# Kernel tuning notes

Hardware: AMD Instinct MI355X
Metric: run time of the kernel (lower is better)

Reference implementation:

```python
import jax, jax.numpy as jnp
import numpy as np

TOPK = 2
NORM_TOPK = True
SCALE = 1.0
EPS = 1e-9


def setup_inputs() -> dict:
    key = jax.random.key(0)
    ks = jax.random.split(key, 9)
    h, i, E = 2048, 1024, 16
    std = 0.02
    return {
        "x": jax.random.normal(ks[0], (1, 2048, h), jnp.float32),
        "Wr": jax.random.normal(ks[1], (E, h), jnp.float32) * std,
        "bias": jnp.zeros((E,), jnp.float32),
        "Wg": jax.random.normal(ks[2], (E, h, i), jnp.float32) * std,
        "Wu": jax.random.normal(ks[3], (E, h, i), jnp.float32) * std,
        "Wd": jax.random.normal(ks[4], (E, i, h), jnp.float32) * std,
        "sWg": jax.random.normal(ks[5], (h, i), jnp.float32) * std,
        "sWu": jax.random.normal(ks[6], (h, i), jnp.float32) * std,
        "sWd": jax.random.normal(ks[7], (i, h), jnp.float32) * std,
    }


def reference(x, Wr, bias, Wg, Wu, Wd, sWg, sWu, sWd):
    b, s, h = x.shape
    E = Wr.shape[0]
    xt = x.reshape(b * s, h)  # [T, h]

    # Router: softmax over expert logits, then top-k
    logits = xt @ Wr.T + bias  # [T, E]
    probs = jax.nn.softmax(logits, axis=-1)
    topk_val, topk_idx = jax.lax.top_k(probs, TOPK)  # [T, K]
    if NORM_TOPK:
        w = topk_val / (jnp.sum(topk_val, axis=-1, keepdims=True) + EPS)
    else:
        w = topk_val
    w = w * SCALE

    # Dense per-expert SwiGLU (mathematically identical to gather/scatter dispatch)
    g = jnp.einsum('th,ehi->tei', xt, Wg)  # [T, E, i]
    u = jnp.einsum('th,ehi->tei', xt, Wu)
    y = jnp.einsum('tei,eih->teh', jax.nn.silu(g) * u, Wd)  # [T, E, h]

    # Combine: out[t] = sum_k w[t,k] * y[t, idx[t,k]]
    oh = jax.nn.one_hot(topk_idx, E, dtype=x.dtype)  # [T, K, E]
    routed = jnp.einsum('tke,tk,teh->th', oh, w, y)

    # Shared expert (SwiGLU)
    shared = (jax.nn.silu(xt @ sWg) * (xt @ sWu)) @ sWd

    return (routed + shared).reshape(b, s, h)
```

## Files before the change

### kernel.cpp

```cpp
#include <hip/hip_runtime.h>
#include <hip/hip_bf16.h>

#define T_TOK 2048
#define HDIM  2048
#define IDIM  1024
#define NE    16
#define NEX   17
#define NASSIGN (T_TOK*3)
#define TM    64

#define G1_NCT 16
#define G2_NCT 32
#define G1_NWG (TM*G1_NCT)
#define G2_NWG (TM*G2_NCT)

typedef __attribute__((ext_vector_type(8))) short bf16x8;
typedef __attribute__((ext_vector_type(4))) float f32x4;

__device__ __forceinline__ unsigned short f2bf(float f) {
    union { float f; unsigned u; } v; v.f = f;
    unsigned r = v.u + 0x7fffu + ((v.u >> 16) & 1u);
    return (unsigned short)(r >> 16);
}
__device__ __forceinline__ unsigned pack2f(float a, float b) {
    __hip_bfloat162 h = __float22bfloat162_rn(float2{a, b});
    unsigned r;
    __builtin_memcpy(&r, &h, 4);
    return r;
}
__device__ __forceinline__ float fidx(const float4& v, int j) {
    return ((const float*)&v)[j];
}
__device__ __forceinline__ int SW(int r) { return (r ^ (r >> 2)) & 7; }
__device__ __forceinline__ int lds_off(int row, int kelem) {
    return (row << 7) + ((((kelem >> 3) ^ SW(row))) << 4) + ((kelem & 7) << 1);
}
__device__ __forceinline__ f32x4 mfma16(bf16x8 a, bf16x8 b, f32x4 c) {
    return __builtin_amdgcn_mfma_f32_16x16x32_bf16(a, b, c, 0, 0, 0);
}

__global__ __launch_bounds__(256) void k_cvt(const float* __restrict__ x,
                                             unsigned short* __restrict__ xbf) {
    int i = blockIdx.x * 256 + threadIdx.x;
    float4 v = ((const float4*)x)[i];
    uint2 p{pack2f(v.x, v.y), pack2f(v.z, v.w)};
    ((uint2*)xbf)[i] = p;
}

__global__ void k_router(const float* __restrict__ x, const float* __restrict__ Wr,
                         const float* __restrict__ bias, float* __restrict__ wtok,
                         int* __restrict__ idxtok, int* __restrict__ counts) {
    int t = blockIdx.x;
    int lane = threadIdx.x & 63;
    int wave = threadIdx.x >> 6;
    __shared__ float lg[NE];
    const float4* xr = (const float4*)(x + (size_t)t * HDIM);
    for (int e = wave; e < NE; e += 4) {
        const float4* wr = (const float4*)(Wr + (size_t)e * HDIM);
        float s = 0.f;
        for (int j = lane; j < HDIM / 4; j += 64) {
            float4 a = xr[j], b = wr[j];
            s += a.x*b.x + a.y*b.y + a.z*b.z + a.w*b.w;
        }
        #pragma unroll
        for (int d = 32; d; d >>= 1) s += __shfl_xor(s, d);
        if (lane == 0) lg[e] = s + bias[e];
    }
    __syncthreads();
    if (threadIdx.x == 0) {
        float m = lg[0];
        #pragma unroll
        for (int e = 1; e < NE; e++) m = fmaxf(m, lg[e]);
        float p[NE]; float S = 0.f;
        #pragma unroll
        for (int e = 0; e < NE; e++) { p[e] = expf(lg[e] - m); S += p[e]; }
        int i0 = 0;
        #pragma unroll
        for (int e = 1; e < NE; e++) if (p[e] > p[i0]) i0 = e;
        int i1 = (i0 == 0) ? 1 : 0;
        for (int e = 0; e < NE; e++) if (e != i0 && p[e] > p[i1]) i1 = e;
        float v0 = p[i0] / S, v1 = p[i1] / S;
        float wsum = v0 + v1 + 1e-9f;
        wtok[t*2+0] = v0 / wsum;
        wtok[t*2+1] = v1 / wsum;
        idxtok[t*2+0] = i0;
        idxtok[t*2+1] = i1;
        atomicAdd(&counts[i0], 1);
        atomicAdd(&counts[i1], 1);
    }
}

__global__ void k_scan(const int* __restrict__ counts, int* __restrict__ offs,
                       int* __restrict__ cursor, int4* __restrict__ tiles) {
    if (threadIdx.x == 0) {
        int acc = 0;
        for (int e = 0; e < NEX; e++) {
            offs[e] = acc; cursor[e] = acc;
            acc += (e < NE) ? counts[e] : T_TOK;
        }
        offs[NEX] = acc;
        int nt = 0;
        for (int e = 0; e < NEX; e++) {
            for (int r = offs[e]; r < offs[e+1]; r += 128) {
                tiles[nt] = int4{r, min(128, offs[e+1] - r), e, 0};
                nt++;
            }
        }
        for (; nt < TM; nt++) tiles[nt] = int4{0, 0, 0, 0};
    }
}

__global__ void k_scatter(const int* __restrict__ idxtok, const float* __restrict__ wtok,
                          int* __restrict__ cursor, const int* __restrict__ offs,
                          int* __restrict__ rows, float* __restrict__ wrow) {
    int t = blockIdx.x * blockDim.x + threadIdx.x;
    if (t >= T_TOK) return;
    #pragma unroll
    for (int k = 0; k < 2; k++) {
        int e = idxtok[t*2+k];
        int pos = atomicAdd(&cursor[e], 1);
        rows[pos] = t;
        wrow[pos] = wtok[t*2+k];
    }
    int p16 = offs[NE] + t;
    rows[p16] = t;
    wrow[p16] = 1.0f;
}

__global__ __launch_bounds__(512) void k_gemm1(
        const unsigned short* __restrict__ xbf,
        const float* __restrict__ Wg, const float* __restrict__ Wu,
        const float* __restrict__ sWg, const float* __restrict__ sWu,
        const int4* __restrict__ tiles, const int* __restrict__ rows,
        const float* __restrict__ wrow, unsigned short* __restrict__ act) {
    int bid = blockIdx.x;
    int wg = (bid & 7) * (G1_NWG >> 3) + (bid >> 3);
    int ti = wg & (TM - 1);
    int ct = wg >> 6;

    int4 tl = tiles[ti];
    int nrows = tl.y;
    if (nrows == 0) return;
    int rs = tl.x, e = tl.z;
    const float* wgp = (e < NE) ? Wg + (size_t)e * HDIM * IDIM : sWg;
    const float* wup = (e < NE) ? Wu + (size_t)e * HDIM * IDIM : sWu;
    int n0 = ct * 64;

    __shared__ unsigned short As[2][128 * 64];
    __shared__ unsigned short Bs[2][64 * 64];
    __shared__ unsigned short Us[2][64 * 64];
    __shared__ int rloc[128];

    int tid = threadIdx.x;
    if (tid < 128) rloc[tid] = rows[rs + min(tid, nrows - 1)];
    __syncthreads();

    int arow = tid >> 2;
    int akc  = (tid & 3) << 4;
    const unsigned short* asrc = xbf + (size_t)rloc[arow] * HDIM + akc;
    int n4 = (tid & 15) << 2;
    int kb = (tid >> 4) << 1;
    const float* gsrc = wgp + (size_t)kb * IDIM + n0 + n4;
    const float* usrc = wup + (size_t)kb * IDIM + n0 + n4;

    int l = tid & 63, w = tid >> 6;
    int wr = (w >> 2) << 6;
    int wc = (w & 3) << 4;
    int fr = l & 15;
    int fk = (l >> 4) << 3;

    uint4 aR0, aR1;
    float4 gR0, gR1, uR0, uR1;

    #define G1_LOAD(K0) do { \
        aR0 = *(const uint4*)(asrc + (K0)); \
        aR1 = *(const uint4*)(asrc + (K0) + 8); \
        gR0 = *(const float4*)(gsrc + (size_t)(K0) * IDIM); \
        gR1 = *(const float4*)(gsrc + (size_t)(K0) * IDIM + IDIM); \
        uR0 = *(const float4*)(usrc + (size_t)(K0) * IDIM); \
        uR1 = *(const float4*)(usrc + (size_t)(K0) * IDIM + IDIM); \
    } while (0)

    #define G1_WRITE(B) do { \
        *(uint4*)((char*)As[B] + lds_off(arow, akc))     = aR0; \
        *(uint4*)((char*)As[B] + lds_off(arow, akc + 8)) = aR1; \
        _Pragma("unroll") \
        for (int i = 0; i < 4; ++i) { \
            int n = n4 + i; \
            *(unsigned*)((char*)Bs[B] + lds_off(n, kb)) = pack2f(fidx(gR0,i), fidx(gR1,i)); \
            *(unsigned*)((char*)Us[B] + lds_off(n, kb)) = pack2f(fidx(uR0,i), fidx(uR1,i)); \
        } \
    } while (0)

    f32x4 accg[4] = {}, accu[4] = {};
    const int NK = HDIM / 64;

    G1_LOAD(0);
    G1_WRITE(0);
    G1_LOAD(64);
    __syncthreads();

    for (int k = 0; k < NK; ++k) {
        int buf = k & 1;
        #pragma unroll
        for (int kh = 0; kh < 2; ++kh) {
            int kk = (kh << 5) + fk;
            bf16x8 a[4], bg, bu;
            #pragma unroll
            for (int m = 0; m < 4; ++m)
                a[m] = *(const bf16x8*)((const char*)As[buf] + lds_off(wr + m * 16 + fr, kk));
            bg = *(const bf16x8*)((const char*)Bs[buf] + lds_off(wc + fr, kk));
            bu = *(const bf16x8*)((const char*)Us[buf] + lds_off(wc + fr, kk));
            #pragma unroll
            for (int m = 0; m < 4; ++m) {
                accg[m] = mfma16(a[m], bg, accg[m]);
                accu[m] = mfma16(a[m], bu, accu[m]);
            }
        }
        if (k + 1 < NK) {
            G1_WRITE(buf ^ 1);
            if (k + 2 < NK) G1_LOAD((k + 2) * 64);
            __syncthreads();
        }
    }

    int crow = (l >> 4) << 2;
    int ccol = l & 15;
    #pragma unroll
    for (int m = 0; m < 4; ++m) {
        #pragma unroll
        for (int reg = 0; reg < 4; ++reg) {
            int r = wr + m * 16 + crow + reg;
            if (r < nrows) {
                float wv = wrow[rs + r];
                float g = accg[m][reg], u = accu[m][reg];
                act[(size_t)(rs + r) * IDIM + n0 + wc + ccol] =
                    f2bf(g / (1.f + __expf(-g)) * u * wv);
            }
        }
    }
}

__global__ __launch_bounds__(512) void k_gemm2(
        const unsigned short* __restrict__ act,
        const float* __restrict__ Wd, const float* __restrict__ sWd,
        const int4* __restrict__ tiles, const int* __restrict__ rows,
        float* __restrict__ out) {
    int bid = blockIdx.x;
    int wg = (bid & 7) * (G2_NWG >> 3) + (bid >> 3);
    int ti = wg & (TM - 1);
    int ct = wg >> 6;

    int4 tl = tiles[ti];
    int nrows = tl.y;
    if (nrows == 0) return;
    int rs = tl.x, e = tl.z;
    const float* wdp = (e < NE) ? Wd + (size_t)e * IDIM * HDIM : sWd;
    int n0 = ct * 64;

    __shared__ unsigned short As[2][128 * 64];
    __shared__ unsigned short Bs[2][64 * 64];
    __shared__ int rloc[128];

    int tid = threadIdx.x;
    if (tid < 128) rloc[tid] = rows[rs + min(tid, nrows - 1)];
    __syncthreads();

    int arow = tid >> 2;
    int akc  = (tid & 3) << 4;
    const unsigned short* asrc = act + (size_t)(rs + min(arow, nrows - 1)) * IDIM + akc;
    int n4 = (tid & 15) << 2;
    int kb = (tid >> 4) << 1;
    const float* dsrc = wdp + (size_t)kb * HDIM + n0 + n4;

    int l = tid & 63, w = tid >> 6;
    int wr = (w >> 2) << 6;
    int wc = (w & 3) << 4;
    int fr = l & 15;
    int fk = (l >> 4) << 3;

    uint4 aR0, aR1;
    float4 dR0, dR1;

    #define G2_LOAD(K0) do { \
        aR0 = *(const uint4*)(asrc + (K0)); \
        aR1 = *(const uint4*)(asrc + (K0) + 8); \
        dR0 = *(const float4*)(dsrc + (size_t)(K0) * HDIM); \
        dR1 = *(const float4*)(dsrc + (size_t)(K0) * HDIM + HDIM); \
    } while (0)

    #define G2_WRITE(B) do { \
        *(uint4*)((char*)As[B] + lds_off(arow, akc))     = aR0; \
        *(uint4*)((char*)As[B] + lds_off(arow, akc + 8)) = aR1; \
        _Pragma("unroll") \
        for (int i = 0; i < 4; ++i) { \
            int n = n4 + i; \
            *(unsigned*)((char*)Bs[B] + lds_off(n, kb)) = pack2f(fidx(dR0,i), fidx(dR1,i)); \
        } \
    } while (0)

    f32x4 acc[4] = {};
    const int NK = IDIM / 64;

    G2_LOAD(0);
    G2_WRITE(0);
    G2_LOAD(64);
    __syncthreads();

    for (int k = 0; k < NK; ++k) {
        int buf = k & 1;
        #pragma unroll
        for (int kh = 0; kh < 2; ++kh) {
            int kk = (kh << 5) + fk;
            bf16x8 a[4], b;
            #pragma unroll
            for (int m = 0; m < 4; ++m)
                a[m] = *(const bf16x8*)((const char*)As[buf] + lds_off(wr + m * 16 + fr, kk));
            b = *(const bf16x8*)((const char*)Bs[buf] + lds_off(wc + fr, kk));
            #pragma unroll
            for (int m = 0; m < 4; ++m)
                acc[m] = mfma16(a[m], b, acc[m]);
        }
        if (k + 1 < NK) {
            G2_WRITE(buf ^ 1);
            if (k + 2 < NK) G2_LOAD((k + 2) * 64);
            __syncthreads();
        }
    }

    int crow = (l >> 4) << 2;
    int ccol = l & 15;
    #pragma unroll
    for (int m = 0; m < 4; ++m) {
        #pragma unroll
        for (int reg = 0; reg < 4; ++reg) {
            int r = wr + m * 16 + crow + reg;
            if (r < nrows) {
                atomicAdd(&out[(size_t)rloc[r] * HDIM + n0 + wc + ccol], acc[m][reg]);
            }
        }
    }
}

extern "C" void kernel_launch(void* const* d_in, const int* in_sizes, int n_in,
                              void* d_out, int out_size, void* d_ws, size_t ws_size,
                              hipStream_t stream) {
    const float* x    = (const float*)d_in[0];
    const float* Wr   = (const float*)d_in[1];
    const float* bias = (const float*)d_in[2];
    const float* Wg   = (const float*)d_in[3];
    const float* Wu   = (const float*)d_in[4];
    const float* Wd   = (const float*)d_in[5];
    const float* sWg  = (const float*)d_in[6];
    const float* sWu  = (const float*)d_in[7];
    const float* sWd  = (const float*)d_in[8];
    float* out = (float*)d_out;

    char* p = (char*)d_ws;
    int*   counts = (int*)p;                 p += 256;
    int*   offs   = (int*)p;                 p += 256;
    int*   cursor = (int*)p;                 p += 256;
    int4*  tiles  = (int4*)p;                p += TM * sizeof(int4);
    int*   idxtok = (int*)p;                 p += (size_t)T_TOK * 2 * sizeof(int);
    float* wtok   = (float*)p;               p += (size_t)T_TOK * 2 * sizeof(float);
    int*   rows   = (int*)p;                 p += (size_t)NASSIGN * sizeof(int);
    float* wrow   = (float*)p;               p += (size_t)NASSIGN * sizeof(float);
    unsigned short* act = (unsigned short*)p; p += (size_t)NASSIGN * IDIM * sizeof(unsigned short);
    unsigned short* xbf = (unsigned short*)p;

    hipMemsetAsync(counts, 0, 256, stream);
    hipMemsetAsync(d_out, 0, (size_t)out_size * sizeof(float), stream);

    k_cvt<<<dim3(T_TOK * HDIM / 1024), dim3(256), 0, stream>>>(x, xbf);
    k_router<<<dim3(T_TOK), dim3(256), 0, stream>>>(x, Wr, bias, wtok, idxtok, counts);
    k_scan<<<dim3(1), dim3(64), 0, stream>>>(counts, offs, cursor, tiles);
    k_scatter<<<dim3((T_TOK + 255) / 256), dim3(256), 0, stream>>>(idxtok, wtok, cursor, offs, rows, wrow);
    k_gemm1<<<dim3(G1_NWG), dim3(512), 0, stream>>>(xbf, Wg, Wu, sWg, sWu, tiles, rows, wrow, act);
    k_gemm2<<<dim3(G2_NWG), dim3(512), 0, stream>>>(act, Wd, sWd, tiles, rows, out);
}
```

Baseline: 318.6 us.

## Load activation tiles directly into LDS with global_load_lds and manual waitcnt pipelining

```diff
diff --git a/kernel.cpp b/kernel.cpp
--- a/kernel.cpp
+++ b/kernel.cpp
@@ -17,6 +17,11 @@
 typedef __attribute__((ext_vector_type(8))) short bf16x8;
 typedef __attribute__((ext_vector_type(4))) float f32x4;
 
+#define WAITVM(N) asm volatile("s_waitcnt vmcnt(" #N ")" ::: "memory")
+#define WAITLGKM  asm volatile("s_waitcnt lgkmcnt(0)" ::: "memory")
+#define SCHEDB    __builtin_amdgcn_sched_barrier(0)
+#define BARRIER   __builtin_amdgcn_s_barrier()
+
 __device__ __forceinline__ unsigned short f2bf(float f) {
     union { float f; unsigned u; } v; v.f = f;
     unsigned r = v.u + 0x7fffu + ((v.u >> 16) & 1u);
@@ -37,6 +42,11 @@
 }
 __device__ __forceinline__ f32x4 mfma16(bf16x8 a, bf16x8 b, f32x4 c) {
     return __builtin_amdgcn_mfma_f32_16x16x32_bf16(a, b, c, 0, 0, 0);
+}
+__device__ __forceinline__ void gload_lds16(const void* g, void* lds) {
+    __builtin_amdgcn_global_load_lds(
+        (const __attribute__((address_space(1))) unsigned*)g,
+        (__attribute__((address_space(3))) unsigned*)lds, 16, 0, 0);
 }
 
 __global__ __launch_bounds__(256) void k_cvt(const float* __restrict__ x,
@@ -155,35 +165,37 @@
     if (tid < 128) rloc[tid] = rows[rs + min(tid, nrows - 1)];
     __syncthreads();
 
-    int arow = tid >> 2;
-    int akc  = (tid & 3) << 4;
-    const unsigned short* asrc = xbf + (size_t)rloc[arow] * HDIM + akc;
+    int l = tid & 63, w = tid >> 6;
+    int ar0 = w * 8 + (l >> 3);
+    int ar1 = 64 + ar0;
+    const unsigned short* asrc0 = xbf + (size_t)rloc[ar0] * HDIM + (((l & 7) ^ SW(ar0)) << 3);
+    const unsigned short* asrc1 = xbf + (size_t)rloc[ar1] * HDIM + (((l & 7) ^ SW(ar1)) << 3);
+
     int n4 = (tid & 15) << 2;
     int kb = (tid >> 4) << 1;
     const float* gsrc = wgp + (size_t)kb * IDIM + n0 + n4;
     const float* usrc = wup + (size_t)kb * IDIM + n0 + n4;
 
-    int l = tid & 63, w = tid >> 6;
     int wr = (w >> 2) << 6;
     int wc = (w & 3) << 4;
     int fr = l & 15;
     int fk = (l >> 4) << 3;
 
-    uint4 aR0, aR1;
     float4 gR0, gR1, uR0, uR1;
 
-    #define G1_LOAD(K0) do { \
-        aR0 = *(const uint4*)(asrc + (K0)); \
-        aR1 = *(const uint4*)(asrc + (K0) + 8); \
+    #define G1_LOADW(K0) do { \
         gR0 = *(const float4*)(gsrc + (size_t)(K0) * IDIM); \
         gR1 = *(const float4*)(gsrc + (size_t)(K0) * IDIM + IDIM); \
         uR0 = *(const float4*)(usrc + (size_t)(K0) * IDIM); \
         uR1 = *(const float4*)(usrc + (size_t)(K0) * IDIM + IDIM); \
     } while (0)
 
-    #define G1_WRITE(B) do { \
-        *(uint4*)((char*)As[B] + lds_off(arow, akc))     = aR0; \
-        *(uint4*)((char*)As[B] + lds_off(arow, akc + 8)) = aR1; \
+    #define G1_GLOADA(K0, B) do { \
+        gload_lds16(asrc0 + (K0), (char*)As[B] + w * 1024); \
+        gload_lds16(asrc1 + (K0), (char*)As[B] + 8192 + w * 1024); \
+    } while (0)
+
+    #define G1_WRITEW(B) do { \
         _Pragma("unroll") \
         for (int i = 0; i < 4; ++i) { \
             int n = n4 + i; \
@@ -194,14 +206,29 @@
 
     f32x4 accg[4] = {}, accu[4] = {};
     const int NK = HDIM / 64;
-
-    G1_LOAD(0);
-    G1_WRITE(0);
-    G1_LOAD(64);
-    __syncthreads();
+    const int KLAST = (NK - 1) * 64;
+
+    G1_LOADW(0);
+    G1_GLOADA(0, 0);
+    SCHEDB;
+    WAITVM(2);
+    G1_WRITEW(0);
+    G1_LOADW(64);
+    SCHEDB;
+    WAITVM(4);
+    WAITLGKM;
+    BARRIER;
 
     for (int k = 0; k < NK; ++k) {
         int buf = k & 1;
+        int kA = min((k + 1) * 64, KLAST);
+        int kW = min((k + 2) * 64, KLAST);
+        G1_GLOADA(kA, buf ^ 1);
+        SCHEDB;
+        WAITVM(2);
+        G1_WRITEW(buf ^ 1);
+        G1_LOADW(kW);
+        SCHEDB;
         #pragma unroll
         for (int kh = 0; kh < 2; ++kh) {
             int kk = (kh << 5) + fk;
@@ -217,12 +244,11 @@
                 accu[m] = mfma16(a[m], bu, accu[m]);
             }
         }
-        if (k + 1 < NK) {
-            G1_WRITE(buf ^ 1);
-            if (k + 2 < NK) G1_LOAD((k + 2) * 64);
-            __syncthreads();
-        }
-    }
+        WAITVM(4);
+        WAITLGKM;
+        BARRIER;
+    }
+    WAITVM(0);
 
     int crow = (l >> 4) << 2;
     int ccol = l & 15;
@@ -239,6 +265,9 @@
             }
         }
     }
+    #undef G1_LOADW
+    #undef G1_GLOADA
+    #undef G1_WRITEW
 }
 
 __global__ __launch_bounds__(512) void k_gemm2(
@@ -266,32 +295,34 @@
     if (tid < 128) rloc[tid] = rows[rs + min(tid, nrows - 1)];
     __syncthreads();
 
-    int arow = tid >> 2;
-    int akc  = (tid & 3) << 4;
-    const unsigned short* asrc = act + (size_t)(rs + min(arow, nrows - 1)) * IDIM + akc;
+    int l = tid & 63, w = tid >> 6;
+    int ar0 = w * 8 + (l >> 3);
+    int ar1 = 64 + ar0;
+    const unsigned short* asrc0 = act + (size_t)(rs + ar0) * IDIM + (((l & 7) ^ SW(ar0)) << 3);
+    const unsigned short* asrc1 = act + (size_t)(rs + ar1) * IDIM + (((l & 7) ^ SW(ar1)) << 3);
+
     int n4 = (tid & 15) << 2;
     int kb = (tid >> 4) << 1;
     const float* dsrc = wdp + (size_t)kb * HDIM + n0 + n4;
 
-    int l = tid & 63, w = tid >> 6;
     int wr = (w >> 2) << 6;
     int wc = (w & 3) << 4;
     int fr = l & 15;
     int fk = (l >> 4) << 3;
 
-    uint4 aR0, aR1;
     float4 dR0, dR1;
 
-    #define G2_LOAD(K0) do { \
-        aR0 = *(const uint4*)(asrc + (K0)); \
-        aR1 = *(const uint4*)(asrc + (K0) + 8); \
+    #define G2_LOADW(K0) do { \
         dR0 = *(const float4*)(dsrc + (size_t)(K0) * HDIM); \
         dR1 = *(const float4*)(dsrc + (size_t)(K0) * HDIM + HDIM); \
     } while (0)
 
-    #define G2_WRITE(B) do { \
-        *(uint4*)((char*)As[B] + lds_off(arow, akc))     = aR0; \
-        *(uint4*)((char*)As[B] + lds_off(arow, akc + 8)) = aR1; \
+    #define G2_GLOADA(K0, B) do { \
+        gload_lds16(asrc0 + (K0), (char*)As[B] + w * 1024); \
+        gload_lds16(asrc1 + (K0), (char*)As[B] + 8192 + w * 1024); \
+    } while (0)
+
+    #define G2_WRITEW(B) do { \
         _Pragma("unroll") \
         for (int i = 0; i < 4; ++i) { \
             int n = n4 + i; \
@@ -301,14 +332,29 @@
 
     f32x4 acc[4] = {};
     const int NK = IDIM / 64;
-
-    G2_LOAD(0);
-    G2_WRITE(0);
-    G2_LOAD(64);
-    __syncthreads();
+    const int KLAST = (NK - 1) * 64;
+
+    G2_LOADW(0);
+    G2_GLOADA(0, 0);
+    SCHEDB;
+    WAITVM(2);
+    G2_WRITEW(0);
+    G2_LOADW(64);
+    SCHEDB;
+    WAITVM(2);
+    WAITLGKM;
+    BARRIER;
 
     for (int k = 0; k < NK; ++k) {
         int buf = k & 1;
+        int kA = min((k + 1) * 64, KLAST);
+        int kW = min((k + 2) * 64, KLAST);
+        G2_GLOADA(kA, buf ^ 1);
+        SCHEDB;
+        WAITVM(2);
+        G2_WRITEW(buf ^ 1);
+        G2_LOADW(kW);
+        SCHEDB;
         #pragma unroll
         for (int kh = 0; kh < 2; ++kh) {
             int kk = (kh << 5) + fk;
@@ -321,12 +367,11 @@
             for (int m = 0; m < 4; ++m)
                 acc[m] = mfma16(a[m], b, acc[m]);
         }
-        if (k + 1 < NK) {
-            G2_WRITE(buf ^ 1);
-            if (k + 2 < NK) G2_LOAD((k + 2) * 64);
-            __syncthreads();
-        }
-    }
+        WAITVM(2);
+        WAITLGKM;
+        BARRIER;
+    }
+    WAITVM(0);
 
     int crow = (l >> 4) << 2;
     int ccol = l & 15;
@@ -340,6 +385,9 @@
             }
         }
     }
+    #undef G2_LOADW
+    #undef G2_GLOADA
+    #undef G2_WRITEW
 }
 
 extern "C" void kernel_launch(void* const* d_in, const int* in_sizes, int n_in,
```

Result: slower. 325.4 us (+2.1%).

## Stream activation tiles via global_load_lds and halve K-tile to 32

Applied to the files above, without the earlier changes.

```diff
diff --git a/kernel.cpp b/kernel.cpp
--- a/kernel.cpp
+++ b/kernel.cpp
@@ -9,10 +9,8 @@
 #define NASSIGN (T_TOK*3)
 #define TM    64
 
-#define G1_NCT 16
-#define G2_NCT 32
-#define G1_NWG (TM*G1_NCT)
-#define G2_NWG (TM*G2_NCT)
+#define G1_NWG (TM*16)
+#define G2_NWG (TM*32)
 
 typedef __attribute__((ext_vector_type(8))) short bf16x8;
 typedef __attribute__((ext_vector_type(4))) float f32x4;
@@ -28,15 +26,17 @@
     __builtin_memcpy(&r, &h, 4);
     return r;
 }
-__device__ __forceinline__ float fidx(const float4& v, int j) {
-    return ((const float*)&v)[j];
-}
-__device__ __forceinline__ int SW(int r) { return (r ^ (r >> 2)) & 7; }
-__device__ __forceinline__ int lds_off(int row, int kelem) {
-    return (row << 7) + ((((kelem >> 3) ^ SW(row))) << 4) + ((kelem & 7) << 1);
+__device__ __forceinline__ int SW2(int r) { return (r >> 1) & 3; }
+__device__ __forceinline__ int lds_off32(int row, int kelem) {
+    return (row << 6) + ((((kelem >> 3) ^ SW2(row))) << 4) + ((kelem & 7) << 1);
 }
 __device__ __forceinline__ f32x4 mfma16(bf16x8 a, bf16x8 b, f32x4 c) {
     return __builtin_amdgcn_mfma_f32_16x16x32_bf16(a, b, c, 0, 0, 0);
+}
+__device__ __forceinline__ void gload_lds16(const void* g, void* lds) {
+    __builtin_amdgcn_global_load_lds(
+        (const __attribute__((address_space(1))) unsigned*)g,
+        (__attribute__((address_space(3))) unsigned*)lds, 16, 0, 0);
 }
 
 __global__ __launch_bounds__(256) void k_cvt(const float* __restrict__ x,
@@ -146,82 +146,78 @@
     const float* wup = (e < NE) ? Wu + (size_t)e * HDIM * IDIM : sWu;
     int n0 = ct * 64;
 
-    __shared__ unsigned short As[2][128 * 64];
-    __shared__ unsigned short Bs[2][64 * 64];
-    __shared__ unsigned short Us[2][64 * 64];
+    __shared__ unsigned short As[2][128 * 32];
+    __shared__ unsigned short Bs[2][64 * 32];
+    __shared__ unsigned short Us[2][64 * 32];
     __shared__ int rloc[128];
 
     int tid = threadIdx.x;
     if (tid < 128) rloc[tid] = rows[rs + min(tid, nrows - 1)];
     __syncthreads();
 
-    int arow = tid >> 2;
-    int akc  = (tid & 3) << 4;
-    const unsigned short* asrc = xbf + (size_t)rloc[arow] * HDIM + akc;
-    int n4 = (tid & 15) << 2;
-    int kb = (tid >> 4) << 1;
-    const float* gsrc = wgp + (size_t)kb * IDIM + n0 + n4;
-    const float* usrc = wup + (size_t)kb * IDIM + n0 + n4;
-
     int l = tid & 63, w = tid >> 6;
+    int arow = w * 16 + (l >> 2);
+    const unsigned short* asrc =
+        xbf + (size_t)rloc[arow] * HDIM + (((l & 3) ^ SW2(arow)) << 3);
+
+    int n2 = (tid & 31) << 1;
+    int kb = (tid >> 5) << 1;
+    const float* gsrc = wgp + (size_t)kb * IDIM + n0 + n2;
+    const float* usrc = wup + (size_t)kb * IDIM + n0 + n2;
+    int wo0 = lds_off32(n2, kb);
+    int wo1 = lds_off32(n2 + 1, kb);
+
     int wr = (w >> 2) << 6;
     int wc = (w & 3) << 4;
     int fr = l & 15;
     int fk = (l >> 4) << 3;
 
-    uint4 aR0, aR1;
-    float4 gR0, gR1, uR0, uR1;
-
-    #define G1_LOAD(K0) do { \
-        aR0 = *(const uint4*)(asrc + (K0)); \
-        aR1 = *(const uint4*)(asrc + (K0) + 8); \
-        gR0 = *(const float4*)(gsrc + (size_t)(K0) * IDIM); \
-        gR1 = *(const float4*)(gsrc + (size_t)(K0) * IDIM + IDIM); \
-        uR0 = *(const float4*)(usrc + (size_t)(K0) * IDIM); \
-        uR1 = *(const float4*)(usrc + (size_t)(K0) * IDIM + IDIM); \
-    } while (0)
-
-    #define G1_WRITE(B) do { \
-        *(uint4*)((char*)As[B] + lds_off(arow, akc))     = aR0; \
-        *(uint4*)((char*)As[B] + lds_off(arow, akc + 8)) = aR1; \
-        _Pragma("unroll") \
-        for (int i = 0; i < 4; ++i) { \
-            int n = n4 + i; \
-            *(unsigned*)((char*)Bs[B] + lds_off(n, kb)) = pack2f(fidx(gR0,i), fidx(gR1,i)); \
-            *(unsigned*)((char*)Us[B] + lds_off(n, kb)) = pack2f(fidx(uR0,i), fidx(uR1,i)); \
-        } \
-    } while (0)
-
+    float2 g0, g1, u0, u1;
     f32x4 accg[4] = {}, accu[4] = {};
-    const int NK = HDIM / 64;
-
-    G1_LOAD(0);
-    G1_WRITE(0);
-    G1_LOAD(64);
+    const int NK = HDIM / 32;
+
+    #define G1_LOADW(KE) do { \
+        const float* gp_ = gsrc + (size_t)(KE) * 32 * IDIM; \
+        const float* up_ = usrc + (size_t)(KE) * 32 * IDIM; \
+        g0 = *(const float2*)(gp_); \
+        g1 = *(const float2*)(gp_ + IDIM); \
+        u0 = *(const float2*)(up_); \
+        u1 = *(const float2*)(up_ + IDIM); \
+    } while (0)
+    #define G1_WRITEW(B) do { \
+        *(unsigned*)((char*)Bs[B] + wo0) = pack2f(g0.x, g1.x); \
+        *(unsigned*)((char*)Bs[B] + wo1) = pack2f(g0.y, g1.y); \
+        *(unsigned*)((char*)Us[B] + wo0) = pack2f(u0.x, u1.x); \
+        *(unsigned*)((char*)Us[B] + wo1) = pack2f(u0.y, u1.y); \
+    } while (0)
+    #define G1_MFMA(B) do { \
+        bf16x8 a0 = *(const bf16x8*)((const char*)As[B] + lds_off32(wr + fr, fk)); \
+        bf16x8 a1 = *(const bf16x8*)((const char*)As[B] + lds_off32(wr + 16 + fr, fk)); \
+        bf16x8 a2 = *(const bf16x8*)((const char*)As[B] + lds_off32(wr + 32 + fr, fk)); \
+        bf16x8 a3 = *(const bf16x8*)((const char*)As[B] + lds_off32(wr + 48 + fr, fk)); \
+        bf16x8 bg = *(const bf16x8*)((const char*)Bs[B] + lds_off32(wc + fr, fk)); \
+        bf16x8 bu = *(const bf16x8*)((const char*)Us[B] + lds_off32(wc + fr, fk)); \
+        accg[0] = mfma16(a0, bg, accg[0]);  accu[0] = mfma16(a0, bu, accu[0]); \
+        accg[1] = mfma16(a1, bg, accg[1]);  accu[1] = mfma16(a1, bu, accu[1]); \
+        accg[2] = mfma16(a2, bg, accg[2]);  accu[2] = mfma16(a2, bu, accu[2]); \
+        accg[3] = mfma16(a3, bg, accg[3]);  accu[3] = mfma16(a3, bu, accu[3]); \
+    } while (0)
+
+    G1_LOADW(0);
+    G1_WRITEW(0);
+    gload_lds16(asrc, (char*)As[0] + w * 1024);
+    G1_LOADW(1);
     __syncthreads();
 
     for (int k = 0; k < NK; ++k) {
         int buf = k & 1;
-        #pragma unroll
-        for (int kh = 0; kh < 2; ++kh) {
-            int kk = (kh << 5) + fk;
-            bf16x8 a[4], bg, bu;
-            #pragma unroll
-            for (int m = 0; m < 4; ++m)
-                a[m] = *(const bf16x8*)((const char*)As[buf] + lds_off(wr + m * 16 + fr, kk));
-            bg = *(const bf16x8*)((const char*)Bs[buf] + lds_off(wc + fr, kk));
-            bu = *(const bf16x8*)((const char*)Us[buf] + lds_off(wc + fr, kk));
-            #pragma unroll
-            for (int m = 0; m < 4; ++m) {
-                accg[m] = mfma16(a[m], bg, accg[m]);
-                accu[m] = mfma16(a[m], bu, accu[m]);
-            }
-        }
         if (k + 1 < NK) {
-            G1_WRITE(buf ^ 1);
-            if (k + 2 < NK) G1_LOAD((k + 2) * 64);
-            __syncthreads();
-        }
+            G1_WRITEW(buf ^ 1);
+            gload_lds16(asrc + (k + 1) * 32, (char*)As[buf ^ 1] + w * 1024);
+            G1_LOADW(min(k + 2, NK - 1));
+        }
+        G1_MFMA(buf);
+        __syncthreads();
     }
 
     int crow = (l >> 4) << 2;
@@ -239,6 +235,9 @@
             }
         }
     }
+    #undef G1_LOADW
+    #undef G1_WRITEW
+    #undef G1_MFMA
 }
 
 __global__ __launch_bounds__(512) void k_gemm2(
@@ -258,74 +257,66 @@
     const float* wdp = (e < NE) ? Wd + (size_t)e * IDIM * HDIM : sWd;
     int n0 = ct * 64;
 
-    __shared__ unsigned short As[2][128 * 64];
-    __shared__ unsigned short Bs[2][64 * 64];
-    __shared__ int rloc[128];
+    __shared__ unsigned short As[2][128 * 32];
+    __shared__ unsigned short Bs[2][64 * 32];
 
     int tid = threadIdx.x;
-    if (tid < 128) rloc[tid] = rows[rs + min(tid, nrows - 1)];
-    __syncthreads();
-
-    int arow = tid >> 2;
-    int akc  = (tid & 3) << 4;
-    const unsigned short* asrc = act + (size_t)(rs + min(arow, nrows - 1)) * IDIM + akc;
-    int n4 = (tid & 15) << 2;
-    int kb = (tid >> 4) << 1;
-    const float* dsrc = wdp + (size_t)kb * HDIM + n0 + n4;
-
     int l = tid & 63, w = tid >> 6;
+    int arow = w * 16 + (l >> 2);
+    const unsigned short* asrc =
+        act + (size_t)(rs + min(arow, nrows - 1)) * IDIM + (((l & 3) ^ SW2(arow)) << 3);
+
+    int n2 = (tid & 31) << 1;
+    int kb = (tid >> 5) << 1;
+    const float* dsrc = wdp + (size_t)kb * HDIM + n0 + n2;
+    int wo0 = lds_off32(n2, kb);
+    int wo1 = lds_off32(n2 + 1, kb);
+
     int wr = (w >> 2) << 6;
     int wc = (w & 3) << 4;
     int fr = l & 15;
     int fk = (l >> 4) << 3;
 
-    uint4 aR0, aR1;
-    float4 dR0, dR1;
-
-    #define G2_LOAD(K0) do { \
-        aR0 = *(const uint4*)(asrc + (K0)); \
-        aR1 = *(const uint4*)(asrc + (K0) + 8); \
-        dR0 = *(const float4*)(dsrc + (size_t)(K0) * HDIM); \
-        dR1 = *(const float4*)(dsrc + (size_t)(K0) * HDIM + HDIM); \
-    } while (0)
-
-    #define G2_WRITE(B) do { \
-        *(uint4*)((char*)As[B] + lds_off(arow, akc))     = aR0; \
-        *(uint4*)((char*)As[B] + lds_off(arow, akc + 8)) = aR1; \
-        _Pragma("unroll") \
-        for (int i = 0; i < 4; ++i) { \
-            int n = n4 + i; \
-            *(unsigned*)((char*)Bs[B] + lds_off(n, kb)) = pack2f(fidx(dR0,i), fidx(dR1,i)); \
-        } \
-    } while (0)
-
+    float2 d0, d1;
     f32x4 acc[4] = {};
-    const int NK = IDIM / 64;
-
-    G2_LOAD(0);
-    G2_WRITE(0);
-    G2_LOAD(64);
+    const int NK = IDIM / 32;
+
+    #define G2_LOADW(KE) do { \
+        const float* dp_ = dsrc + (size_t)(KE) * 32 * HDIM; \
+        d0 = *(const float2*)(dp_); \
+        d1 = *(const float2*)(dp_ + HDIM); \
+    } while (0)
+    #define G2_WRITEW(B) do { \
+        *(unsigned*)((char*)Bs[B] + wo0) = pack2f(d0.x, d1.x); \
+        *(unsigned*)((char*)Bs[B] + wo1) = pack2f(d0.y, d1.y); \
+    } while (0)
+    #define G2_MFMA(B) do { \
+        bf16x8 a0 = *(const bf16x8*)((const char*)As[B] + lds_off32(wr + fr, fk)); \
+        bf16x8 a1 = *(const bf16x8*)((const char*)As[B] + lds_off32(wr + 16 + fr, fk)); \
+        bf16x8 a2 = *(const bf16x8*)((const char*)As[B] + lds_off32(wr + 32 + fr, fk)); \
+        bf16x8 a3 = *(const bf16x8*)((const char*)As[B] + lds_off32(wr + 48 + fr, fk)); \
+        bf16x8 b  = *(const bf16x8*)((const char*)Bs[B] + lds_off32(wc + fr, fk)); \
+        acc[0] = mfma16(a0, b, acc[0]); \
+        acc[1] = mfma16(a1, b, acc[1]); \
+        acc[2] = mfma16(a2, b, acc[2]); \
+        acc[3] = mfma16(a3, b, acc[3]); \
+    } while (0)
+
+    G2_LOADW(0);
+    G2_WRITEW(0);
+    gload_lds16(asrc, (char*)As[0] + w * 1024);
+    G2_LOADW(1);
     __syncthreads();
 
     for (int k = 0; k < NK; ++k) {
         int buf = k & 1;
-        #pragma unroll
-        for (int kh = 0; kh < 2; ++kh) {
-            int kk = (kh << 5) + fk;
-            bf16x8 a[4], b;
-            #pragma unroll
-            for (int m = 0; m < 4; ++m)
-                a[m] = *(const bf16x8*)((const char*)As[buf] + lds_off(wr + m * 16 + fr, kk));
-            b = *(const bf16x8*)((const char*)Bs[buf] + lds_off(wc + fr, kk));
-            #pragma unroll
-            for (int m = 0; m < 4; ++m)
-                acc[m] = mfma16(a[m], b, acc[m]);
-        }
         if (k + 1 < NK) {
-            G2_WRITE(buf ^ 1);
-            if (k + 2 < NK) G2_LOAD((k + 2) * 64);
-            __syncthreads();
-        }
+            G2_WRITEW(buf ^ 1);
+            gload_lds16(asrc + (k + 1) * 32, (char*)As[buf ^ 1] + w * 1024);
+            G2_LOADW(min(k + 2, NK - 1));
+        }
+        G2_MFMA(buf);
+        __syncthreads();
     }
 
     int crow = (l >> 4) << 2;
@@ -336,10 +327,13 @@
         for (int reg = 0; reg < 4; ++reg) {
             int r = wr + m * 16 + crow + reg;
             if (r < nrows) {
-                atomicAdd(&out[(size_t)rloc[r] * HDIM + n0 + wc + ccol], acc[m][reg]);
+                atomicAdd(&out[(size_t)rows[rs + r] * HDIM + n0 + wc + ccol], acc[m][reg]);
             }
         }
     }
+    #undef G2_LOADW
+    #undef G2_WRITEW
+    #undef G2_MFMA
 }
 
 extern "C" void kernel_launch(void* const* d_in, const int* in_sizes, int n_in,
```

Measured after the change: 416.2 us. 1.31x slower.
